# Optimization experiments

Hardware: AMD Instinct MI355X
Metric: run time of the kernel (lower is better)

Reference implementation:

```python
import jax, jax.numpy as jnp
import numpy as np

N, E, H = 50000, 800000, 128
HQ = H // 4  # 32


def _mlp(x, w1, b1, w2, b2):
    return jax.nn.relu(x @ w1 + b1) @ w2 + b2


def setup_inputs() -> dict:
    key = jax.random.key(0)
    ks = jax.random.split(key, 16)

    def lin(k, fan_in, fan_out):
        lim = 1.0 / np.sqrt(fan_in)
        kw, kb = jax.random.split(k)
        w = jax.random.uniform(kw, (fan_in, fan_out), jnp.float32, -lim, lim)
        b = jax.random.uniform(kb, (fan_out,), jnp.float32, -lim, lim)
        return w, b

    x = jax.random.normal(ks[0], (N, H), jnp.float32)
    pos = jax.random.normal(ks[1], (N, 3), jnp.float32)
    edge_index = jax.random.randint(ks[2], (2, E), 0, N, jnp.int64)

    pw1, pb1 = lin(ks[3], 3, HQ)
    pw2, pb2 = lin(ks[4], HQ, HQ)
    mw1, mb1 = lin(ks[5], 2 * H + HQ, H)
    mw2, mb2 = lin(ks[6], H, H)
    uw1, ub1 = lin(ks[7], 2 * H, H)
    uw2, ub2 = lin(ks[8], H, H)

    return dict(x=x, pos=pos, edge_index=edge_index,
                pw1=pw1, pb1=pb1, pw2=pw2, pb2=pb2,
                mw1=mw1, mb1=mb1, mw2=mw2, mb2=mb2,
                uw1=uw1, ub1=ub1, uw2=uw2, ub2=ub2)


def reference(x, pos, edge_index,
              pw1, pb1, pw2, pb2,
              mw1, mb1, mw2, mb2,
              uw1, ub1, uw2, ub2):
    row, col = edge_index[0], edge_index[1]
    # position features from relative positions [E, 3] -> [E, H//4]
    pos_feat = _mlp(pos[row] - pos[col], pw1, pb1, pw2, pb2)
    # per-edge messages [E, 2H + H//4] -> [E, H]
    msg_in = jnp.concatenate([x[row], x[col], pos_feat], axis=-1)
    messages = _mlp(msg_in, mw1, mb1, mw2, mb2)
    # scatter-add messages into destination nodes (index_add on col)
    agg = jax.ops.segment_sum(messages, col, num_segments=x.shape[0])
    # node update [N, 2H] -> [N, H]
    return _mlp(jnp.concatenate([x, agg], axis=-1), uw1, ub1, uw2, ub2)
```

## Files before the change

kernel.cpp:

```cpp
#include <hip/hip_runtime.h>
#include <hip/hip_bf16.h>

#define NN 50000
#define NE 800000
#define HD 128
#define SCAN_CHUNK 1024
#define SCAN_BLOCKS ((NN + SCAN_CHUNK - 1) / SCAN_CHUNK)

typedef __attribute__((ext_vector_type(8))) short s16x8;
typedef __attribute__((ext_vector_type(4))) float f32x4;

static __device__ __forceinline__ unsigned short f2bf(float f) {
    unsigned int u = __float_as_uint(f);
    u = (u + 0x7FFFu + ((u >> 16) & 1u)) >> 16;
    return (unsigned short)u;
}
static __device__ __forceinline__ float bf2f(unsigned short h) {
    return __uint_as_float(((unsigned int)h) << 16);
}
static __device__ __forceinline__ unsigned int f2bf2(float lo, float hi) {
    __hip_bfloat162 h = __float22bfloat162_rn(make_float2(lo, hi));
    return *reinterpret_cast<unsigned int*>(&h);
}

#define WFENCE() do { asm volatile("s_waitcnt lgkmcnt(0)" ::: "memory"); \
                      __builtin_amdgcn_sched_barrier(0); } while (0)

__global__ void hist_kernel(const int* __restrict__ ei, int* __restrict__ cnt)
{
    __shared__ int sIdx64;
    if (threadIdx.x == 0) {
        int z = 1;
        for (int k = 0; k < 16; ++k) if (ei[2 * k + 1] != 0) z = 0;
        sIdx64 = z;
    }
    __syncthreads();
    int g = blockIdx.x * 256 + threadIdx.x;
    if (g >= NE / 2) return;
    int e0 = g * 2;
    int c0, c1;
    if (sIdx64) { int4 q = *(const int4*)&ei[2 * NE + 2 * e0]; c0 = q.x; c1 = q.z; }
    else        { int2 q = *(const int2*)&ei[NE + e0];         c0 = q.x; c1 = q.y; }
    atomicAdd(&cnt[c0], 1);
    atomicAdd(&cnt[c1], 1);
}

__global__ void scan1_kernel(const int* __restrict__ cnt, int* __restrict__ cursor,
                             int* __restrict__ bsum)
{
    __shared__ int tot[256];
    int b = blockIdx.x, t = threadIdx.x;
    int i0 = b * SCAN_CHUNK + t * 4;
    int v[4];
    #pragma unroll
    for (int k = 0; k < 4; ++k) v[k] = (i0 + k < NN) ? cnt[i0 + k] : 0;
    tot[t] = v[0] + v[1] + v[2] + v[3];
    __syncthreads();
    if (t == 0) {
        int run = 0;
        for (int i = 0; i < 256; ++i) { int x = tot[i]; tot[i] = run; run += x; }
        bsum[b] = run;
    }
    __syncthreads();
    int p = tot[t];
    #pragma unroll
    for (int k = 0; k < 4; ++k) {
        if (i0 + k < NN) cursor[i0 + k] = p;
        p += v[k];
    }
}

__global__ void scan3_kernel(int* __restrict__ cursor, const int* __restrict__ bsum)
{
    __shared__ int sCarry;
    int b = blockIdx.x, t = threadIdx.x;
    if (t == 0) {
        int run = 0;
        for (int i = 0; i < b; ++i) run += bsum[i];
        sCarry = run;
    }
    __syncthreads();
    int carry = sCarry;
    int i0 = b * SCAN_CHUNK + t * 4;
    #pragma unroll
    for (int k = 0; k < 4; ++k)
        if (i0 + k < NN) cursor[i0 + k] += carry;
}

__global__ void scatter_kernel(const int* __restrict__ ei,
                               int* __restrict__ cursor, int2* __restrict__ sRC)
{
    __shared__ int sIdx64;
    if (threadIdx.x == 0) {
        int z = 1;
        for (int k = 0; k < 16; ++k) if (ei[2 * k + 1] != 0) z = 0;
        sIdx64 = z;
    }
    __syncthreads();
    int g = blockIdx.x * 256 + threadIdx.x;
    if (g >= NE / 2) return;
    int e0 = g * 2;
    int r0, r1, c0, c1;
    if (sIdx64) {
        int4 qr = *(const int4*)&ei[2 * e0];           r0 = qr.x; r1 = qr.z;
        int4 qc = *(const int4*)&ei[2 * NE + 2 * e0];  c0 = qc.x; c1 = qc.z;
    } else {
        int2 qr = *(const int2*)&ei[e0];       r0 = qr.x; r1 = qr.y;
        int2 qc = *(const int2*)&ei[NE + e0];  c0 = qc.x; c1 = qc.y;
    }
    int p0 = atomicAdd(&cursor[c0], 1);
    sRC[p0] = make_int2(r0, c0);
    int p1 = atomicAdd(&cursor[c1], 1);
    sRC[p1] = make_int2(r1, c1);
}

__global__ void prepall_kernel(const float* __restrict__ pw2, const float* __restrict__ pb2,
                               const float* __restrict__ mw1, const float* __restrict__ mb1,
                               const float* __restrict__ mw2, const float* __restrict__ mb2,
                               const float* __restrict__ uw1,
                               float* __restrict__ Wpc, float* __restrict__ bc,
                               float* __restrict__ W3, float* __restrict__ b3)
{
    int tid = threadIdx.x;
    if (blockIdx.x == 64) {
        for (int idx = tid; idx < 32 * 128; idx += 256) {
            int j = idx >> 7, k = idx & 127;
            float s = 0.f;
            #pragma unroll 8
            for (int i = 0; i < 32; ++i) s += pw2[j * 32 + i] * mw1[(256 + i) * 128 + k];
            Wpc[idx] = s;
        }
        if (tid < 128) {
            float s = mb1[tid];
            #pragma unroll 8
            for (int i = 0; i < 32; ++i) s += pb2[i] * mw1[(256 + i) * 128 + tid];
            bc[tid] = s;
        }
        return;
    }
    int idx = blockIdx.x * 256 + tid;
    {
        int k = idx >> 7, j = idx & 127;
        float s = 0.f;
        #pragma unroll 4
        for (int c = 0; c < 128; ++c)
            s += mw2[k * 128 + c] * uw1[(128 + c) * 128 + j];
        W3[idx] = s;
    }
    if (blockIdx.x == 0 && tid < 128) {
        int j = tid;
        float s = 0.f;
        #pragma unroll 4
        for (int c = 0; c < 128; ++c)
            s += mb2[c] * uw1[(128 + c) * 128 + j];
        b3[j] = s;
    }
}

__global__ __launch_bounds__(256, 3) void node_kernel(
    const float* __restrict__ x, const float* __restrict__ mw1,
    const float* __restrict__ bcv,
    unsigned short* __restrict__ xa, unsigned short* __restrict__ xb,
    float* __restrict__ aggH)
{
    __shared__ __align__(16) unsigned short sB[128 * 136];
    __shared__ __align__(16) unsigned short sSt[4][16 * 132];

    int tid = threadIdx.x;
    {
        f32x4 z = {0.f, 0.f, 0.f, 0.f};
        const int total4 = NN * HD / 4;
        for (int i = blockIdx.x * 256 + tid; i < total4; i += gridDim.x * 256)
            ((f32x4*)aggH)[i] = z;
    }
    int half = blockIdx.x & 1;
    for (int idx = tid; idx < 128 * 128; idx += 256) {
        int c = idx & 127, k = idx >> 7;
        sB[c * 136 + k] = f2bf(mw1[(half * 128 + k) * 128 + c]);
    }
    __syncthreads();

    int lane = tid & 63, wv = tid >> 6;
    int r16 = lane & 15, g4 = lane >> 4;
    unsigned short* st = sSt[wv];
    unsigned short* dst = half ? xb : xa;
    float bcr[8];
    #pragma unroll
    for (int tc = 0; tc < 8; ++tc) bcr[tc] = half ? bcv[tc * 16 + r16] : 0.f;
    const int NT = NN / 16;
    const int nb = gridDim.x >> 1;
    const int bid = blockIdx.x >> 1;

    for (int t = bid * 4 + wv; t < NT; t += nb * 4) {
        int r0 = t * 16;
        int row = r0 + r16;
        s16x8 a[4];
        #pragma unroll
        for (int ks = 0; ks < 4; ++ks) {
            const float* p = &x[(size_t)row * HD + ks * 32 + g4 * 8];
            float4 v0 = *(const float4*)p;
            float4 v1 = *(const float4*)(p + 4);
            union { s16x8 v; unsigned int u[4]; } av;
            av.u[0] = f2bf2(v0.x, v0.y); av.u[1] = f2bf2(v0.z, v0.w);
            av.u[2] = f2bf2(v1.x, v1.y); av.u[3] = f2bf2(v1.z, v1.w);
            a[ks] = av.v;
        }
        float hold[4];
        #pragma unroll
        for (int tc = 0; tc < 8; ++tc) {
            int col = tc * 16 + r16;
            float bv = bcr[tc];
            f32x4 acc = {bv, bv, bv, bv};
            #pragma unroll
            for (int ks = 0; ks < 4; ++ks) {
                s16x8 b = *(const s16x8*)&sB[col * 136 + ks * 32 + g4 * 8];
                acc = __builtin_amdgcn_mfma_f32_16x16x32_bf16(a[ks], b, acc, 0, 0, 0);
            }
            if ((tc & 1) == 0) {
                #pragma unroll
                for (int j = 0; j < 4; ++j) hold[j] = acc[j];
            } else {
                #pragma unroll
                for (int j = 0; j < 4; ++j)
                    *(unsigned int*)&st[(g4 * 4 + j) * 132 + r16 * 8 + (tc - 1)] =
                        f2bf2(hold[j], acc[j]);
            }
        }
        WFENCE();
        #pragma unroll
        for (int i = 0; i < 4; ++i) {
            int idx = i * 512 + lane * 8;
            int rr = idx >> 7, cc = idx & 127;
            *(s16x8*)&dst[(size_t)(r0 + rr) * HD + cc] = *(const s16x8*)&st[rr * 132 + cc];
        }
        WFENCE();
    }
}

__global__ __launch_bounds__(256, 3) void edge_kernel(
    const float* __restrict__ pos, const int2* __restrict__ sRC,
    const float* __restrict__ pw1, const float* __restrict__ pb1,
    const unsigned short* __restrict__ xa, const unsigned short* __restrict__ xb,
    const float* __restrict__ Wpc,
    float* __restrict__ aggH)
{
    __shared__ __align__(16) unsigned short sT[4][16 * 136];
    __shared__ int sECs[4][16];

    int tid = threadIdx.x;
    int lane = tid & 63, wv = tid >> 6;
    int r16 = lane & 15, g4 = lane >> 4;
    unsigned short* stg = sT[wv];
    int* secw = sECs[wv];

    s16x8 wr[8];
    #pragma unroll
    for (int tc = 0; tc < 8; ++tc) {
        s16x8 w;
        #pragma unroll
        for (int i = 0; i < 8; ++i)
            w[i] = (short)f2bf(Wpc[(g4 * 8 + i) * 128 + tc * 16 + r16]);
        wr[tc] = w;
    }
    float pw10[8], pw11[8], pw12[8], pb1r[8];
    #pragma unroll
    for (int i = 0; i < 8; ++i) {
        int k = g4 * 8 + i;
        pw10[i] = pw1[k]; pw11[i] = pw1[32 + k]; pw12[i] = pw1[64 + k];
        pb1r[i] = pb1[k];
    }

    const int NW = gridDim.x * 4;
    const int NT = NE / 16;
    int gw = blockIdx.x * 4 + wv;
    if (gw >= NT) return;

    int2 rc = sRC[gw * 16 + r16];
    int2 rcN = rc;
    if (gw + NW < NT) rcN = sRC[(gw + NW) * 16 + r16];
    float dp0 = pos[rc.x * 3 + 0] - pos[rc.y * 3 + 0];
    float dp1 = pos[rc.x * 3 + 1] - pos[rc.y * 3 + 1];
    float dp2 = pos[rc.x * 3 + 2] - pos[rc.y * 3 + 2];
    s16x8 ga[4], gb[4];
    #pragma unroll
    for (int j = 0; j < 4; ++j) {
        int gx = __shfl(rc.x, g4 * 4 + j, 64);
        int gy = __shfl(rc.y, g4 * 4 + j, 64);
        ga[j] = *(const s16x8*)&xa[(size_t)gx * HD + r16 * 8];
        gb[j] = *(const s16x8*)&xb[(size_t)gy * HD + r16 * 8];
    }

    for (int t = gw; t < NT; t += NW) {
        bool hn  = (t + NW) < NT;
        bool hn2 = (t + 2 * NW) < NT;

        if (lane < 16) secw[lane] = rc.y;
        union { s16x8 v; unsigned int u[4]; } apf;
        #pragma unroll
        for (int i2 = 0; i2 < 4; ++i2) {
            int i = 2 * i2;
            float v0 = fmaf(dp0, pw10[i], fmaf(dp1, pw11[i], fmaf(dp2, pw12[i], pb1r[i])));
            float v1 = fmaf(dp0, pw10[i+1], fmaf(dp1, pw11[i+1], fmaf(dp2, pw12[i+1], pb1r[i+1])));
            apf.u[i2] = f2bf2(fmaxf(v0, 0.f), fmaxf(v1, 0.f));
        }

        float hold[4];
        #pragma unroll
        for (int tc = 0; tc < 8; ++tc) {
            f32x4 acc;
            #pragma unroll
            for (int j = 0; j < 4; ++j)
                acc[j] = bf2f((unsigned short)ga[j][tc]) + bf2f((unsigned short)gb[j][tc]);
            acc = __builtin_amdgcn_mfma_f32_16x16x32_bf16(apf.v, wr[tc], acc, 0, 0, 0);
            if ((tc & 1) == 0) {
                #pragma unroll
                for (int j = 0; j < 4; ++j) hold[j] = fmaxf(acc[j], 0.f);
            } else {
                #pragma unroll
                for (int j = 0; j < 4; ++j)
                    *(unsigned int*)&stg[(g4 * 4 + j) * 136 + r16 * 8 + (tc - 1)] =
                        f2bf2(hold[j], fmaxf(acc[j], 0.f));
            }
        }
        WFENCE();

        if (hn) {
            #pragma unroll
            for (int j = 0; j < 4; ++j) {
                int gx = __shfl(rcN.x, g4 * 4 + j, 64);
                int gy = __shfl(rcN.y, g4 * 4 + j, 64);
                ga[j] = *(const s16x8*)&xa[(size_t)gx * HD + r16 * 8];
                gb[j] = *(const s16x8*)&xb[(size_t)gy * HD + r16 * 8];
            }
        }

        int2 rcN2 = rcN;
        if (hn2) rcN2 = sRC[(t + 2 * NW) * 16 + r16];
        float dp0N = 0.f, dp1N = 0.f, dp2N = 0.f;
        if (hn) {
            dp0N = pos[rcN.x * 3 + 0] - pos[rcN.y * 3 + 0];
            dp1N = pos[rcN.x * 3 + 1] - pos[rcN.y * 3 + 1];
            dp2N = pos[rcN.x * 3 + 2] - pos[rcN.y * 3 + 2];
        }

        {
            int p0 = (lane & 15) * 8 + (lane >> 4);
            int p1 = p0 + 4;
            int cur = secw[0];
            float run0 = bf2f(stg[p0]);
            float run1 = bf2f(stg[p1]);
            #pragma unroll
            for (int e = 1; e < 16; ++e) {
                int c = secw[e];
                float v0 = bf2f(stg[e * 136 + p0]);
                float v1 = bf2f(stg[e * 136 + p1]);
                if (c != cur) {
                    unsafeAtomicAdd(&aggH[(size_t)cur * HD + lane], run0);
                    unsafeAtomicAdd(&aggH[(size_t)cur * HD + lane + 64], run1);
                    cur = c; run0 = v0; run1 = v1;
                } else { run0 += v0; run1 += v1; }
            }
            unsafeAtomicAdd(&aggH[(size_t)cur * HD + lane], run0);
            unsafeAtomicAdd(&aggH[(size_t)cur * HD + lane + 64], run1);
        }
        WFENCE();

        rc = rcN; rcN = rcN2; dp0 = dp0N; dp1 = dp1N; dp2 = dp2N;
    }
}

__global__ __launch_bounds__(768, 1) void upd_kernel(
    const float* __restrict__ x, const float* __restrict__ aggH,
    const int* __restrict__ cnt,
    const float* __restrict__ uw1, const float* __restrict__ ub1,
    const float* __restrict__ W3, const float* __restrict__ b3,
    const float* __restrict__ uw2, const float* __restrict__ ub2,
    float* __restrict__ out)
{
    __shared__ __align__(16) unsigned short sB1a[128 * 136];
    __shared__ __align__(16) unsigned short sW3l[128 * 136];
    __shared__ __align__(16) unsigned short sB2[128 * 136];
    __shared__ __align__(16) unsigned short sSt[12][16 * 136];

    int tid = threadIdx.x;
    for (int idx = tid; idx < 128 * 128; idx += 768) {
        int c = idx & 127, k = idx >> 7;
        sB1a[c * 136 + k] = f2bf(uw1[k * 128 + c]);
        sW3l[c * 136 + k] = f2bf(W3[k * 128 + c]);
        sB2[c * 136 + k]  = f2bf(uw2[k * 128 + c]);
    }
    __syncthreads();

    int lane = tid & 63, wv = tid >> 6;
    int r16 = lane & 15, g4 = lane >> 4;
    unsigned short* st = sSt[wv];
    float ub1r[8], ub2r[8], b3r[8];
    #pragma unroll
    for (int tc = 0; tc < 8; ++tc) {
        ub1r[tc] = ub1[tc * 16 + r16];
        ub2r[tc] = ub2[tc * 16 + r16];
        b3r[tc]  = b3[tc * 16 + r16];
    }

    const int NT = NN / 16;
    for (int t = blockIdx.x * 12 + wv; t < NT; t += gridDim.x * 12) {
        int r0 = t * 16;
        int row = r0 + r16;
        s16x8 a[8];
        #pragma unroll
        for (int ks = 0; ks < 8; ++ks) {
            const float* p = (ks < 4) ? &x[(size_t)row * HD + ks * 32 + g4 * 8]
                                      : &aggH[(size_t)row * HD + (ks - 4) * 32 + g4 * 8];
            float4 v0 = *(const float4*)p;
            float4 v1 = *(const float4*)(p + 4);
            union { s16x8 v; unsigned int u[4]; } av;
            av.u[0] = f2bf2(v0.x, v0.y); av.u[1] = f2bf2(v0.z, v0.w);
            av.u[2] = f2bf2(v1.x, v1.y); av.u[3] = f2bf2(v1.z, v1.w);
            a[ks] = av.v;
        }
        float cn[4];
        #pragma unroll
        for (int j = 0; j < 4; ++j) cn[j] = (float)cnt[r0 + g4 * 4 + j];

        #pragma unroll
        for (int tc = 0; tc < 8; ++tc) {
            int col = tc * 16 + r16;
            f32x4 acc;
            #pragma unroll
            for (int j = 0; j < 4; ++j) acc[j] = ub1r[tc] + cn[j] * b3r[tc];
            #pragma unroll
            for (int ks = 0; ks < 4; ++ks) {
                s16x8 b = *(const s16x8*)&sB1a[col * 136 + ks * 32 + g4 * 8];
                acc = __builtin_amdgcn_mfma_f32_16x16x32_bf16(a[ks], b, acc, 0, 0, 0);
            }
            #pragma unroll
            for (int ks = 4; ks < 8; ++ks) {
                s16x8 b = *(const s16x8*)&sW3l[col * 136 + (ks - 4) * 32 + g4 * 8];
                acc = __builtin_amdgcn_mfma_f32_16x16x32_bf16(a[ks], b, acc, 0, 0, 0);
            }
            #pragma unroll
            for (int j = 0; j < 4; ++j)
                st[(g4 * 4 + j) * 136 + col] = f2bf(fmaxf(acc[j], 0.f));
        }
        WFENCE();
        s16x8 a2[4];
        #pragma unroll
        for (int ks = 0; ks < 4; ++ks)
            a2[ks] = *(const s16x8*)&st[r16 * 136 + ks * 32 + g4 * 8];
        WFENCE();
        #pragma unroll
        for (int tc = 0; tc < 8; ++tc) {
            int col = tc * 16 + r16;
            float bv = ub2r[tc];
            f32x4 acc = {bv, bv, bv, bv};
            #pragma unroll
            for (int ks = 0; ks < 4; ++ks) {
                s16x8 b = *(const s16x8*)&sB2[col * 136 + ks * 32 + g4 * 8];
                acc = __builtin_amdgcn_mfma_f32_16x16x32_bf16(a2[ks], b, acc, 0, 0, 0);
            }
            #pragma unroll
            for (int j = 0; j < 4; ++j)
                out[(size_t)(r0 + g4 * 4 + j) * HD + col] = acc[j];
        }
    }
}

extern "C" void kernel_launch(void* const* d_in, const int* in_sizes, int n_in,
                              void* d_out, int out_size, void* d_ws, size_t ws_size,
                              hipStream_t stream)
{
    const float* x   = (const float*)d_in[0];
    const float* pos = (const float*)d_in[1];
    const int*   ei  = (const int*)d_in[2];
    const float* pw1 = (const float*)d_in[3];
    const float* pb1 = (const float*)d_in[4];
    const float* pw2 = (const float*)d_in[5];
    const float* pb2 = (const float*)d_in[6];
    const float* mw1 = (const float*)d_in[7];
    const float* mb1 = (const float*)d_in[8];
    const float* mw2 = (const float*)d_in[9];
    const float* mb2 = (const float*)d_in[10];
    const float* uw1 = (const float*)d_in[11];
    const float* ub1 = (const float*)d_in[12];
    const float* uw2 = (const float*)d_in[13];
    const float* ub2 = (const float*)d_in[14];
    float* out = (float*)d_out;

    char* ws = (char*)d_ws;
    float*          aggH   = (float*)(ws);
    unsigned short* xa     = (unsigned short*)(ws + 25600000);
    unsigned short* xb     = (unsigned short*)(ws + 38400000);
    float*          Wpc    = (float*)(ws + 51200000);
    float*          bcv    = (float*)(ws + 51216384);
    int*            cnt    = (int*)(ws + 51216896);
    int*            cursor = (int*)(ws + 51417600);
    int*            bsum   = (int*)(ws + 51618304);
    int2*           sRC    = (int2*)(ws + 51618560);

    float* W3 = (float*)(ws + 51417600);
    float* b3 = (float*)(ws + 51417600 + 65536);

    hipMemsetAsync(cnt, 0, NN * sizeof(int), stream);
    hist_kernel<<<(NE / 2 + 255) / 256, 256, 0, stream>>>(ei, cnt);
    scan1_kernel<<<SCAN_BLOCKS, 256, 0, stream>>>(cnt, cursor, bsum);
    scan3_kernel<<<SCAN_BLOCKS, 256, 0, stream>>>(cursor, bsum);
    scatter_kernel<<<(NE / 2 + 255) / 256, 256, 0, stream>>>(ei, cursor, sRC);
    prepall_kernel<<<65, 256, 0, stream>>>(pw2, pb2, mw1, mb1, mw2, mb2, uw1,
                                           Wpc, bcv, W3, b3);
    node_kernel<<<1024, 256, 0, stream>>>(x, mw1, bcv, xa, xb, aggH);
    edge_kernel<<<768, 256, 0, stream>>>(pos, sRC, pw1, pb1, xa, xb, Wpc, aggH);
    upd_kernel<<<256, 768, 0, stream>>>(x, aggH, cnt, uw1, ub1, W3, b3, uw2, ub2, out);
}
```

Measured before the change: 229.7 us.

## Merge histogram, weight prep and node projection into one heterogeneous setup kernel

Combines hist, prepall and node kernels into a single launch where block ranges do different jobs: node projection with aggH zeroing, edge-count histogram, and weight pre-products. Each node-half block now computes the folded bias from mb1, pb2 and mw1 inline, so the node work no longer depends on prepall. W3/b3 move to their own workspace region, since they previously aliased cursor. The aim is to cut two launch gaps and let the small histogram and prep work overlap the node GEMM. In exchange, block specialisation may hurt occupancy balance, the node path now uses the 256-thread bounds, and every node-half block repeats the bias computation.

Result: no change. 232.2 us (+1.1%).

```diff
diff --git a/kernel.cpp b/kernel.cpp
--- a/kernel.cpp
+++ b/kernel.cpp
@@ -6,6 +6,9 @@
 #define HD 128
 #define SCAN_CHUNK 1024
 #define SCAN_BLOCKS ((NN + SCAN_CHUNK - 1) / SCAN_CHUNK)
+#define NB_NODE 1024
+#define NB_HIST ((NE / 2 + 255) / 256)
+#define NB_PREP 65
 
 typedef __attribute__((ext_vector_type(8))) short s16x8;
 typedef __attribute__((ext_vector_type(4))) float f32x4;
@@ -26,23 +29,153 @@
 #define WFENCE() do { asm volatile("s_waitcnt lgkmcnt(0)" ::: "memory"); \
                       __builtin_amdgcn_sched_barrier(0); } while (0)
 
-__global__ void hist_kernel(const int* __restrict__ ei, int* __restrict__ cnt)
-{
+__global__ __launch_bounds__(256, 3) void setup_kernel(
+    const float* __restrict__ x, const float* __restrict__ mw1,
+    const float* __restrict__ mb1,
+    const float* __restrict__ pw2, const float* __restrict__ pb2,
+    const float* __restrict__ mw2, const float* __restrict__ mb2,
+    const float* __restrict__ uw1, const int* __restrict__ ei,
+    unsigned short* __restrict__ xa, unsigned short* __restrict__ xb,
+    float* __restrict__ aggH, int* __restrict__ cnt,
+    float* __restrict__ Wpc, float* __restrict__ W3, float* __restrict__ b3)
+{
+    __shared__ __align__(16) unsigned short sB[128 * 136];
+    __shared__ __align__(16) unsigned short sSt[4][16 * 132];
     __shared__ int sIdx64;
-    if (threadIdx.x == 0) {
-        int z = 1;
-        for (int k = 0; k < 16; ++k) if (ei[2 * k + 1] != 0) z = 0;
-        sIdx64 = z;
+
+    int bid = blockIdx.x;
+    int tid = threadIdx.x;
+
+    if (bid >= NB_NODE) {
+        int rb = bid - NB_NODE;
+        if (rb < NB_HIST) {
+            if (tid == 0) {
+                int z = 1;
+                for (int k = 0; k < 16; ++k) if (ei[2 * k + 1] != 0) z = 0;
+                sIdx64 = z;
+            }
+            __syncthreads();
+            int g = rb * 256 + tid;
+            if (g >= NE / 2) return;
+            int e0 = g * 2;
+            int c0, c1;
+            if (sIdx64) { int4 q = *(const int4*)&ei[2 * NE + 2 * e0]; c0 = q.x; c1 = q.z; }
+            else        { int2 q = *(const int2*)&ei[NE + e0];         c0 = q.x; c1 = q.y; }
+            atomicAdd(&cnt[c0], 1);
+            atomicAdd(&cnt[c1], 1);
+            return;
+        }
+        rb -= NB_HIST;
+        if (rb == 64) {
+            for (int idx = tid; idx < 32 * 128; idx += 256) {
+                int j = idx >> 7, k = idx & 127;
+                float s = 0.f;
+                #pragma unroll 8
+                for (int i = 0; i < 32; ++i) s += pw2[j * 32 + i] * mw1[(256 + i) * 128 + k];
+                Wpc[idx] = s;
+            }
+            return;
+        }
+        int idx = rb * 256 + tid;
+        {
+            int k = idx >> 7, j = idx & 127;
+            float s = 0.f;
+            #pragma unroll 4
+            for (int c = 0; c < 128; ++c)
+                s += mw2[k * 128 + c] * uw1[(128 + c) * 128 + j];
+            W3[idx] = s;
+        }
+        if (rb == 0 && tid < 128) {
+            int j = tid;
+            float s = 0.f;
+            #pragma unroll 4
+            for (int c = 0; c < 128; ++c)
+                s += mb2[c] * uw1[(128 + c) * 128 + j];
+            b3[j] = s;
+        }
+        return;
+    }
+
+    {
+        f32x4 z = {0.f, 0.f, 0.f, 0.f};
+        const int total4 = NN * HD / 4;
+        for (int i = bid * 256 + tid; i < total4; i += NB_NODE * 256)
+            ((f32x4*)aggH)[i] = z;
+    }
+    int half = bid & 1;
+    for (int idx = tid; idx < 128 * 128; idx += 256) {
+        int c = idx & 127, k = idx >> 7;
+        sB[c * 136 + k] = f2bf(mw1[(half * 128 + k) * 128 + c]);
     }
     __syncthreads();
-    int g = blockIdx.x * 256 + threadIdx.x;
-    if (g >= NE / 2) return;
-    int e0 = g * 2;
-    int c0, c1;
-    if (sIdx64) { int4 q = *(const int4*)&ei[2 * NE + 2 * e0]; c0 = q.x; c1 = q.z; }
-    else        { int2 q = *(const int2*)&ei[NE + e0];         c0 = q.x; c1 = q.y; }
-    atomicAdd(&cnt[c0], 1);
-    atomicAdd(&cnt[c1], 1);
+
+    int lane = tid & 63, wv = tid >> 6;
+    int r16 = lane & 15, g4 = lane >> 4;
+    unsigned short* st = sSt[wv];
+    unsigned short* dst = half ? xb : xa;
+
+    float bcr[8];
+    #pragma unroll
+    for (int tc = 0; tc < 8; ++tc) bcr[tc] = 0.f;
+    if (half) {
+        #pragma unroll
+        for (int tc = 0; tc < 8; ++tc) bcr[tc] = mb1[tc * 16 + r16];
+        for (int i = 0; i < 32; ++i) {
+            float pv = pb2[i];
+            #pragma unroll
+            for (int tc = 0; tc < 8; ++tc)
+                bcr[tc] = fmaf(pv, mw1[(256 + i) * 128 + tc * 16 + r16], bcr[tc]);
+        }
+    }
+
+    const int NT = NN / 16;
+    const int nb = NB_NODE >> 1;
+    const int nbid = bid >> 1;
+
+    for (int t = nbid * 4 + wv; t < NT; t += nb * 4) {
+        int r0 = t * 16;
+        int row = r0 + r16;
+        s16x8 a[4];
+        #pragma unroll
+        for (int ks = 0; ks < 4; ++ks) {
+            const float* p = &x[(size_t)row * HD + ks * 32 + g4 * 8];
+            float4 v0 = *(const float4*)p;
+            float4 v1 = *(const float4*)(p + 4);
+            union { s16x8 v; unsigned int u[4]; } av;
+            av.u[0] = f2bf2(v0.x, v0.y); av.u[1] = f2bf2(v0.z, v0.w);
+            av.u[2] = f2bf2(v1.x, v1.y); av.u[3] = f2bf2(v1.z, v1.w);
+            a[ks] = av.v;
+        }
+        float hold[4];
+        #pragma unroll
+        for (int tc = 0; tc < 8; ++tc) {
+            int col = tc * 16 + r16;
+            float bv = bcr[tc];
+            f32x4 acc = {bv, bv, bv, bv};
+            #pragma unroll
+            for (int ks = 0; ks < 4; ++ks) {
+                s16x8 b = *(const s16x8*)&sB[col * 136 + ks * 32 + g4 * 8];
+                acc = __builtin_amdgcn_mfma_f32_16x16x32_bf16(a[ks], b, acc, 0, 0, 0);
+            }
+            if ((tc & 1) == 0) {
+                #pragma unroll
+                for (int j = 0; j < 4; ++j) hold[j] = acc[j];
+            } else {
+                #pragma unroll
+                for (int j = 0; j < 4; ++j)
+                    *(unsigned int*)&st[(g4 * 4 + j) * 132 + r16 * 8 + (tc - 1)] =
+                        f2bf2(hold[j], acc[j]);
+            }
+        }
+        WFENCE();
+        #pragma unroll
+        for (int i = 0; i < 4; ++i) {
+            int idx = i * 512 + lane * 8;
+            int rr = idx >> 7, cc = idx & 127;
+            *(s16x8*)&dst[(size_t)(r0 + rr) * HD + cc] = *(const s16x8*)&st[rr * 132 + cc];
+        }
+        WFENCE();
+    }
 }
 
 __global__ void scan1_kernel(const int* __restrict__ cnt, int* __restrict__ cursor,
@@ -112,129 +245,6 @@
     sRC[p0] = make_int2(r0, c0);
     int p1 = atomicAdd(&cursor[c1], 1);
     sRC[p1] = make_int2(r1, c1);
-}
-
-__global__ void prepall_kernel(const float* __restrict__ pw2, const float* __restrict__ pb2,
-                               const float* __restrict__ mw1, const float* __restrict__ mb1,
-                               const float* __restrict__ mw2, const float* __restrict__ mb2,
-                               const float* __restrict__ uw1,
-                               float* __restrict__ Wpc, float* __restrict__ bc,
-                               float* __restrict__ W3, float* __restrict__ b3)
-{
-    int tid = threadIdx.x;
-    if (blockIdx.x == 64) {
-        for (int idx = tid; idx < 32 * 128; idx += 256) {
-            int j = idx >> 7, k = idx & 127;
-            float s = 0.f;
-            #pragma unroll 8
-            for (int i = 0; i < 32; ++i) s += pw2[j * 32 + i] * mw1[(256 + i) * 128 + k];
-            Wpc[idx] = s;
-        }
-        if (tid < 128) {
-            float s = mb1[tid];
-            #pragma unroll 8
-            for (int i = 0; i < 32; ++i) s += pb2[i] * mw1[(256 + i) * 128 + tid];
-            bc[tid] = s;
-        }
-        return;
-    }
-    int idx = blockIdx.x * 256 + tid;
-    {
-        int k = idx >> 7, j = idx & 127;
-        float s = 0.f;
-        #pragma unroll 4
-        for (int c = 0; c < 128; ++c)
-            s += mw2[k * 128 + c] * uw1[(128 + c) * 128 + j];
-        W3[idx] = s;
-    }
-    if (blockIdx.x == 0 && tid < 128) {
-        int j = tid;
-        float s = 0.f;
-        #pragma unroll 4
-        for (int c = 0; c < 128; ++c)
-            s += mb2[c] * uw1[(128 + c) * 128 + j];
-        b3[j] = s;
-    }
-}
-
-__global__ __launch_bounds__(256, 3) void node_kernel(
-    const float* __restrict__ x, const float* __restrict__ mw1,
-    const float* __restrict__ bcv,
-    unsigned short* __restrict__ xa, unsigned short* __restrict__ xb,
-    float* __restrict__ aggH)
-{
-    __shared__ __align__(16) unsigned short sB[128 * 136];
-    __shared__ __align__(16) unsigned short sSt[4][16 * 132];
-
-    int tid = threadIdx.x;
-    {
-        f32x4 z = {0.f, 0.f, 0.f, 0.f};
-        const int total4 = NN * HD / 4;
-        for (int i = blockIdx.x * 256 + tid; i < total4; i += gridDim.x * 256)
-            ((f32x4*)aggH)[i] = z;
-    }
-    int half = blockIdx.x & 1;
-    for (int idx = tid; idx < 128 * 128; idx += 256) {
-        int c = idx & 127, k = idx >> 7;
-        sB[c * 136 + k] = f2bf(mw1[(half * 128 + k) * 128 + c]);
-    }
-    __syncthreads();
-
-    int lane = tid & 63, wv = tid >> 6;
-    int r16 = lane & 15, g4 = lane >> 4;
-    unsigned short* st = sSt[wv];
-    unsigned short* dst = half ? xb : xa;
-    float bcr[8];
-    #pragma unroll
-    for (int tc = 0; tc < 8; ++tc) bcr[tc] = half ? bcv[tc * 16 + r16] : 0.f;
-    const int NT = NN / 16;
-    const int nb = gridDim.x >> 1;
-    const int bid = blockIdx.x >> 1;
-
-    for (int t = bid * 4 + wv; t < NT; t += nb * 4) {
-        int r0 = t * 16;
-        int row = r0 + r16;
-        s16x8 a[4];
-        #pragma unroll
-        for (int ks = 0; ks < 4; ++ks) {
-            const float* p = &x[(size_t)row * HD + ks * 32 + g4 * 8];
-            float4 v0 = *(const float4*)p;
-            float4 v1 = *(const float4*)(p + 4);
-            union { s16x8 v; unsigned int u[4]; } av;
-            av.u[0] = f2bf2(v0.x, v0.y); av.u[1] = f2bf2(v0.z, v0.w);
-            av.u[2] = f2bf2(v1.x, v1.y); av.u[3] = f2bf2(v1.z, v1.w);
-            a[ks] = av.v;
-        }
-        float hold[4];
-        #pragma unroll
-        for (int tc = 0; tc < 8; ++tc) {
-            int col = tc * 16 + r16;
-            float bv = bcr[tc];
-            f32x4 acc = {bv, bv, bv, bv};
-            #pragma unroll
-            for (int ks = 0; ks < 4; ++ks) {
-                s16x8 b = *(const s16x8*)&sB[col * 136 + ks * 32 + g4 * 8];
-                acc = __builtin_amdgcn_mfma_f32_16x16x32_bf16(a[ks], b, acc, 0, 0, 0);
-            }
-            if ((tc & 1) == 0) {
-                #pragma unroll
-                for (int j = 0; j < 4; ++j) hold[j] = acc[j];
-            } else {
-                #pragma unroll
-                for (int j = 0; j < 4; ++j)
-                    *(unsigned int*)&st[(g4 * 4 + j) * 132 + r16 * 8 + (tc - 1)] =
-                        f2bf2(hold[j], acc[j]);
-            }
-        }
-        WFENCE();
-        #pragma unroll
-        for (int i = 0; i < 4; ++i) {
-            int idx = i * 512 + lane * 8;
-            int rr = idx >> 7, cc = idx & 127;
-            *(s16x8*)&dst[(size_t)(r0 + rr) * HD + cc] = *(const s16x8*)&st[rr * 132 + cc];
-        }
-        WFENCE();
-    }
 }
 
 __global__ __launch_bounds__(256, 3) void edge_kernel(
@@ -491,23 +501,20 @@
     unsigned short* xa     = (unsigned short*)(ws + 25600000);
     unsigned short* xb     = (unsigned short*)(ws + 38400000);
     float*          Wpc    = (float*)(ws + 51200000);
-    float*          bcv    = (float*)(ws + 51216384);
     int*            cnt    = (int*)(ws + 51216896);
     int*            cursor = (int*)(ws + 51417600);
     int*            bsum   = (int*)(ws + 51618304);
     int2*           sRC    = (int2*)(ws + 51618560);
-
-    float* W3 = (float*)(ws + 51417600);
-    float* b3 = (float*)(ws + 51417600 + 65536);
+    float*          W3     = (float*)(ws + 58018560);
+    float*          b3     = (float*)(ws + 58084096);
 
     hipMemsetAsync(cnt, 0, NN * sizeof(int), stream);
-    hist_kernel<<<(NE / 2 + 255) / 256, 256, 0, stream>>>(ei, cnt);
+    setup_kernel<<<NB_NODE + NB_HIST + NB_PREP, 256, 0, stream>>>(
+        x, mw1, mb1, pw2, pb2, mw2, mb2, uw1, ei,
+        xa, xb, aggH, cnt, Wpc, W3, b3);
     scan1_kernel<<<SCAN_BLOCKS, 256, 0, stream>>>(cnt, cursor, bsum);
     scan3_kernel<<<SCAN_BLOCKS, 256, 0, stream>>>(cursor, bsum);
     scatter_kernel<<<(NE / 2 + 255) / 256, 256, 0, stream>>>(ei, cursor, sRC);
-    prepall_kernel<<<65, 256, 0, stream>>>(pw2, pb2, mw1, mb1, mw2, mb2, uw1,
-                                           Wpc, bcv, W3, b3);
-    node_kernel<<<1024, 256, 0, stream>>>(x, mw1, bcv, xa, xb, aggH);
     edge_kernel<<<768, 256, 0, stream>>>(pos, sRC, pw1, pb1, xa, xb, Wpc, aggH);
     upd_kernel<<<256, 768, 0, stream>>>(x, aggH, cnt, uw1, ub1, W3, b3, uw2, ub2, out);
 }
```
